# Performance work log

Measured on AMD Instinct MI355X. Metric: run time of the kernel, lower is better.

## Reference

```python
import jax, jax.numpy as jnp
import numpy as np

K = 20
EPS = 1e-5
NEG_SLOPE = 0.2


def knn(x, k):
    # x: [B, C, N] -> idx [B, N, k] of nearest neighbors (negative sq-dist topk)
    inner = -2.0 * jnp.einsum('bcn,bcm->bnm', x, x)
    xx = jnp.sum(x * x, axis=1)  # [B, N]
    d = -xx[:, :, None] - inner - xx[:, None, :]
    return jax.lax.top_k(d, k)[1]


def get_graph_feature(x, k):
    # x: [B, C, N] -> [B, 2C, N, k]
    idx = knn(x, k)
    xt = jnp.transpose(x, (0, 2, 1))            # [B, N, C]
    feat = jax.vmap(lambda a, i: a[i])(xt, idx)  # [B, N, k, C]
    center = xt[:, :, None, :]
    out = jnp.concatenate([feat - center, jnp.broadcast_to(center, feat.shape)], axis=-1)
    return jnp.transpose(out, (0, 3, 1, 2))


def conv_bn_lrelu(x, w, g, b):
    # 1x1 conv + BatchNorm2d (batch stats, training mode) + LeakyReLU(0.2)
    y = jnp.einsum('oc,bcnk->bonk', w, x)
    mu = jnp.mean(y, axis=(0, 2, 3), keepdims=True)
    var = jnp.mean((y - mu) ** 2, axis=(0, 2, 3), keepdims=True)
    y = (y - mu) * jax.lax.rsqrt(var + EPS)
    y = y * g[None, :, None, None] + b[None, :, None, None]
    return jnp.where(y >= 0, y, NEG_SLOPE * y)


def lrelu(y):
    return jnp.where(y >= 0, y, NEG_SLOPE * y)


def setup_inputs() -> dict:
    key = jax.random.key(0)
    ks = jax.random.split(key, 24)
    B, N = 8, 4096
    d = {}
    d['x'] = jax.random.normal(ks[0], (B, 3, N), dtype=jnp.float32)
    def wconv(k_, o, c):
        return jax.random.normal(k_, (o, c), dtype=jnp.float32) * (1.0 / np.sqrt(c))
    d['w1'] = wconv(ks[1], 32, 6)
    d['g1'] = 1.0 + 0.1 * jax.random.normal(ks[2], (32,), dtype=jnp.float32)
    d['b1'] = 0.1 * jax.random.normal(ks[3], (32,), dtype=jnp.float32)
    d['w2'] = wconv(ks[4], 64, 70)
    d['g2'] = 1.0 + 0.1 * jax.random.normal(ks[5], (64,), dtype=jnp.float32)
    d['b2'] = 0.1 * jax.random.normal(ks[6], (64,), dtype=jnp.float32)
    d['wd1'] = wconv(ks[7], 64, 64)
    d['gd1'] = 1.0 + 0.1 * jax.random.normal(ks[8], (64,), dtype=jnp.float32)
    d['bd1'] = 0.1 * jax.random.normal(ks[9], (64,), dtype=jnp.float32)
    d['wd2'] = wconv(ks[10], 64, 128)
    d['gd2'] = 1.0 + 0.1 * jax.random.normal(ks[11], (64,), dtype=jnp.float32)
    d['bd2'] = 0.1 * jax.random.normal(ks[12], (64,), dtype=jnp.float32)
    d['W2d'] = jax.random.normal(ks[13], (128, 128), dtype=jnp.float32) * (1.0 / np.sqrt(128))
    d['b2d'] = 0.1 * jax.random.normal(ks[14], (128,), dtype=jnp.float32)
    d['W3d'] = jax.random.normal(ks[15], (64, 128), dtype=jnp.float32) * (1.0 / np.sqrt(128))
    d['b3d'] = 0.1 * jax.random.normal(ks[16], (64,), dtype=jnp.float32)
    d['W4d'] = jax.random.normal(ks[17], (11, 64), dtype=jnp.float32) * (1.0 / np.sqrt(64))
    d['b4d'] = 0.1 * jax.random.normal(ks[18], (11,), dtype=jnp.float32)
    return d


def reference(x, w1, g1, b1, w2, g2, b2, wd1, gd1, bd1, wd2, gd2, bd2,
              W2d, b2d, W3d, b3d, W4d, b4d):
    x1_gf = get_graph_feature(x, K)                    # [B, 6, N, k]
    x1_max = jnp.max(conv_bn_lrelu(x1_gf, w1, g1, b1), axis=-1)  # [B, 32, N]
    x2_gf = jnp.concatenate([x1_gf, get_graph_feature(x1_max, K)], axis=1)  # [B, 70, N, k]
    x2_max = jnp.max(conv_bn_lrelu(x2_gf, w2, g2, b2), axis=-1)  # [B, 64, N]
    xd1 = jnp.max(conv_bn_lrelu(get_graph_feature(x1_max, K), wd1, gd1, bd1), axis=-1)  # [B, 64, N]
    xd2 = jnp.max(conv_bn_lrelu(get_graph_feature(x2_max, K), wd2, gd2, bd2), axis=-1)  # [B, 64, N]
    h = jnp.concatenate([xd1, xd2], axis=1)            # [B, 128, N]
    h = h.reshape(1, -1, 128)                          # faithful row-major view
    h = jnp.mean(h, axis=1)                            # [1, 128]
    h = lrelu(h @ W2d.T + b2d)
    h = lrelu(h @ W3d.T + b3d)
    return lrelu(h @ W4d.T + b4d)                      # [1, 11]
```

## Files before the change

kernel.cpp:

```cpp
#include <hip/hip_runtime.h>

#define BB 8
#define NN 4096
#define KK 20
constexpr float EPSV = 1e-5f;
constexpr float SLOPE = 0.2f;

typedef __bf16 bfrag __attribute__((ext_vector_type(8)));
typedef float floatx4 __attribute__((ext_vector_type(4)));
typedef unsigned short us4 __attribute__((ext_vector_type(4)));
typedef unsigned short us8 __attribute__((ext_vector_type(8)));

__device__ __forceinline__ float lrelu(float v) { return v >= 0.f ? v : SLOPE * v; }

__device__ __forceinline__ unsigned short bf16rn(float f) {
    unsigned int u = __float_as_uint(f);
    return (unsigned short)((u + 0x7FFFu + ((u >> 16) & 1u)) >> 16);
}
__device__ __forceinline__ float bf16up(unsigned short h) {
    return __uint_as_float(((unsigned int)h) << 16);
}

__device__ __forceinline__ void gl_lds16(const unsigned short* g, unsigned short* l) {
    __builtin_amdgcn_global_load_lds((const __attribute__((address_space(1))) void*)g,
                                     (__attribute__((address_space(3))) void*)l, 16, 0, 0);
}

__global__ void zero_kernel(float* p, int n) {
    int i = blockIdx.x * 256 + threadIdx.x;
    if (i < n) p[i] = 0.f;
}

__global__ void pack3_kernel(const float* __restrict__ src, unsigned short* __restrict__ pk) {
    const int id = blockIdx.x;
    const int b = id & 7;
    const int m = (id >> 3) * 256 + threadIdx.x;
    us8 w0, w1;
    #pragma unroll
    for (int j = 0; j < 8; j++) { w0[j] = 0; w1[j] = 0; }
    unsigned short row[12];
    float s = 0.f;
    #pragma unroll
    for (int c = 0; c < 3; c++) {
        float v = src[(b * 3 + c) * NN + m];
        s += v * v;
        unsigned short h = bf16rn(v);
        unsigned short l = bf16rn(v - bf16up(h));
        row[c] = h; row[3 + c] = l; row[6 + c] = l; row[9 + c] = h;
    }
    #pragma unroll
    for (int j = 0; j < 8; j++) w0[j] = row[j];
    #pragma unroll
    for (int j = 0; j < 4; j++) w1[j] = row[8 + j];
    unsigned short* dst = pk + (size_t)(b * NN + m) * 40;
    us8 z;
    #pragma unroll
    for (int j = 0; j < 8; j++) z[j] = 0;
    unsigned int ub = __float_as_uint(0.5f * s);
    us8 zh = z;
    zh[0] = (unsigned short)(ub & 0xFFFFu);
    zh[1] = (unsigned short)(ub >> 16);
    *(us8*)(dst) = w0;
    *(us8*)(dst + 8) = w1;
    *(us8*)(dst + 16) = z;
    *(us8*)(dst + 24) = z;
    *(us8*)(dst + 32) = zh;
}

template<int C>
__global__ __launch_bounds__(256) void knn_kernel(const float* __restrict__ src,
                                                  const unsigned short* __restrict__ pk,
                                                  int* __restrict__ idx) {
    constexpr int SK = (C == 3) ? 40 : (2 * C + 8);
    constexpr int HNOFF = (C == 3) ? 32 : 2 * C;
    constexpr int UNITS = 8 * SK;
    constexpr int PF = (UNITS + 255) / 256;
    constexpr int KKN = (C == 3) ? 1 : (C / 32);
    __shared__ __attribute__((aligned(16))) unsigned short cpack[2 * 64 * SK];
    __shared__ float pv[64 * 65];
    __shared__ unsigned short pidx[64 * 66];
    __shared__ float tau[64];
    __shared__ int cnt[64];
    __shared__ unsigned short qls[(C == 3) ? 64 * 40 : 2];

    const int bid = blockIdx.x;
    const int b = bid & 7;
    const int q0 = (bid >> 3) * 64;
    const int tid = threadIdx.x;
    const int lane = tid & 63;
    const int wv = tid >> 6;
    const int wr = (wv >> 1) * 32;
    const int wc = (wv & 1) * 32;
    const int fl = lane & 15;
    const int fq = lane >> 4;

    float tv[20]; int ti[20];
    #pragma unroll
    for (int k = 0; k < 20; k++) { tv[k] = -3.4e38f; ti[k] = 0; }

    bfrag qah[KKN][2], qal[KKN][2];
    if (C == 3) {
        for (int i = tid; i < 64 * 20; i += 256) {
            int r = i / 20, k = 12 + i % 20;
            qls[r * 40 + k] = 0;
        }
        if (tid < 64) {
            #pragma unroll
            for (int c = 0; c < 3; c++) {
                float v = src[(b * 3 + c) * NN + q0 + tid];
                unsigned short h = bf16rn(v);
                unsigned short l = bf16rn(v - bf16up(h));
                qls[tid * 40 + c] = h;  qls[tid * 40 + 3 + c] = l;
                qls[tid * 40 + 6 + c] = h;  qls[tid * 40 + 9 + c] = l;
            }
        }
    } else {
        #pragma unroll
        for (int r2 = 0; r2 < 2; r2++) {
            const unsigned short* qr = pk + (size_t)(b * NN + q0 + wr + r2 * 16 + fl) * SK + fq * 8;
            #pragma unroll
            for (int kk = 0; kk < KKN; kk++) {
                qah[kk][r2] = *(const bfrag*)(qr + kk * 32);
                qal[kk][r2] = *(const bfrag*)(qr + C + kk * 32);
            }
        }
    }

    {
        const unsigned short* p0 = pk + (size_t)(b * NN) * SK;
        #pragma unroll
        for (int r = 0; r < PF; r++) {
            int u0 = r * 256 + wv * 64;
            if (u0 < UNITS)
                gl_lds16(p0 + (size_t)(u0 + lane) * 8, cpack + (size_t)u0 * 8);
        }
    }
    if (tid < 64) { tau[tid] = -3.4e38f; cnt[tid] = 0; }
    __syncthreads();

    bfrag qa3[2];
    if (C == 3) {
        #pragma unroll
        for (int r2 = 0; r2 < 2; r2++)
            qa3[r2] = *(const bfrag*)(&qls[(wr + r2 * 16 + fl) * 40 + fq * 8]);
    }

    int buf = 0;
    for (int ch = 0; ch < 64; ch++) {
        unsigned short* cur = cpack + buf * (64 * SK);
        if (ch + 1 < 64) {
            unsigned short* nxt = cpack + (buf ^ 1) * (64 * SK);
            const unsigned short* pn = pk + (size_t)(b * NN + (ch + 1) * 64) * SK;
            #pragma unroll
            for (int r = 0; r < PF; r++) {
                int u0 = r * 256 + wv * 64;
                if (u0 < UNITS)
                    gl_lds16(pn + (size_t)(u0 + lane) * 8, nxt + (size_t)u0 * 8);
            }
        }

        floatx4 acc[2][2];
        #pragma unroll
        for (int r2 = 0; r2 < 2; r2++)
            #pragma unroll
            for (int c2 = 0; c2 < 2; c2++)
                acc[r2][c2] = (floatx4)(0.f);

        if (C == 3) {
            #pragma unroll
            for (int c2 = 0; c2 < 2; c2++) {
                bfrag bm = *(const bfrag*)(&cur[(wc + c2 * 16 + fl) * SK + fq * 8]);
                #pragma unroll
                for (int r2 = 0; r2 < 2; r2++)
                    acc[r2][c2] = __builtin_amdgcn_mfma_f32_16x16x32_bf16(qa3[r2], bm, acc[r2][c2], 0, 0, 0);
            }
        } else {
            #pragma unroll
            for (int kk = 0; kk < KKN; kk++) {
                const int kb = kk * 32 + fq * 8;
                bfrag bh[2], bl[2];
                #pragma unroll
                for (int c2 = 0; c2 < 2; c2++) {
                    bh[c2] = *(const bfrag*)(&cur[(wc + c2 * 16 + fl) * SK + kb]);
                    bl[c2] = *(const bfrag*)(&cur[(wc + c2 * 16 + fl) * SK + C + kb]);
                }
                #pragma unroll
                for (int r2 = 0; r2 < 2; r2++)
                    #pragma unroll
                    for (int c2 = 0; c2 < 2; c2++) {
                        acc[r2][c2] = __builtin_amdgcn_mfma_f32_16x16x32_bf16(qah[kk][r2], bh[c2], acc[r2][c2], 0, 0, 0);
                        acc[r2][c2] = __builtin_amdgcn_mfma_f32_16x16x32_bf16(qah[kk][r2], bl[c2], acc[r2][c2], 0, 0, 0);
                        acc[r2][c2] = __builtin_amdgcn_mfma_f32_16x16x32_bf16(qal[kk][r2], bh[c2], acc[r2][c2], 0, 0, 0);
                        acc[r2][c2] = __builtin_amdgcn_mfma_f32_16x16x32_bf16(qal[kk][r2], bl[c2], acc[r2][c2], 0, 0, 0);
                    }
            }
        }

        {
            const int m0 = ch * 64;
            float hvv[2];
            #pragma unroll
            for (int c2 = 0; c2 < 2; c2++)
                hvv[c2] = *(const float*)(&cur[(wc + c2 * 16 + fl) * SK + HNOFF]);
            #pragma unroll
            for (int r2 = 0; r2 < 2; r2++) {
                const int qb = wr + r2 * 16 + fq * 4;
                float4 t4 = *(const float4*)(&tau[qb]);
                float ta[4] = { t4.x, t4.y, t4.z, t4.w };
                #pragma unroll
                for (int c2 = 0; c2 < 2; c2++) {
                    const float hv = hvv[c2];
                    const int mm = m0 + wc + c2 * 16 + fl;
                    #pragma unroll
                    for (int reg = 0; reg < 4; reg++) {
                        float s = acc[r2][c2][reg] - hv;
                        if (s > ta[reg]) {
                            int q = qb + reg;
                            int p = atomicAdd(&cnt[q], 1);
                            pv[q * 65 + p] = s;
                            pidx[q * 66 + p] = (unsigned short)mm;
                        }
                    }
                }
            }
        }
        __syncthreads();

        if (tid < 64) {
            int n = cnt[tid];
            for (int t = 0; t < n; t++) {
                float v = pv[tid * 65 + t];
                if (v > tv[0]) {
                    tv[0] = v; ti[0] = (int)pidx[tid * 66 + t];
                    #pragma unroll
                    for (int j = 0; j < 19; j++) {
                        if (tv[j] > tv[j + 1]) {
                            float a = tv[j]; tv[j] = tv[j + 1]; tv[j + 1] = a;
                            int bi = ti[j]; ti[j] = ti[j + 1]; ti[j + 1] = bi;
                        }
                    }
                }
            }
            cnt[tid] = 0;
            tau[tid] = tv[0];
        }
        __syncthreads();
        buf ^= 1;
    }

    if (tid < 64) {
        #pragma unroll
        for (int k = 0; k < 20; k++)
            idx[(b * NN + q0 + tid) * KK + k] = ti[k];
    }
}

template<int COUT>
__global__ void precompute_kernel(const float* __restrict__ src, int C,
                                  const float* __restrict__ w, int CIN, int wd_off, int wc_off,
                                  float* __restrict__ G, float* __restrict__ H) {
    constexpr int MY = 256 / COUT;
    extern __shared__ float lds[];
    float* wd = lds;
    float* wc = lds + C * COUT;
    const int id = blockIdx.x;
    const int b = id & 7;
    const int m_base = (id >> 3) * 64;
    const int tid = threadIdx.y * COUT + threadIdx.x;
    for (int i = tid; i < C * COUT; i += 256) {
        int c = i / COUT, o = i % COUT;
        float a  = w[o * CIN + wd_off + c];
        float cc = w[o * CIN + wc_off + c];
        wd[i] = a;
        wc[i] = cc - a;
    }
    __syncthreads();
    const int o = threadIdx.x;
    for (int it = 0; it < COUT / 4; it++) {
        int m = m_base + it * MY + threadIdx.y;
        float g = 0.f, h = 0.f;
        for (int c = 0; c < C; c++) {
            float s = src[(b * C + c) * NN + m];
            g += wd[c * COUT + o] * s;
            h += wc[c * COUT + o] * s;
        }
        int gi = (b * NN + m) * COUT + o;
        G[gi] = g;
        H[gi] = h;
    }
}

__global__ void precompute2_kernel(const float* __restrict__ srcA, const float* __restrict__ srcB,
                                   const float* __restrict__ w,
                                   float* __restrict__ GA, float* __restrict__ GB,
                                   float* __restrict__ H) {
    constexpr int COUT = 64, CA = 3, CB = 32, CIN = 70;
    __shared__ float wdA[CA * COUT], wcA[CA * COUT], wdB[CB * COUT], wcB[CB * COUT];
    const int id = blockIdx.x;
    const int b = id & 7;
    const int m_base = (id >> 3) * 64;
    const int tid = threadIdx.y * COUT + threadIdx.x;
    for (int i = tid; i < CA * COUT; i += 256) {
        int c = i / COUT, o = i % COUT;
        float a = w[o * CIN + 0 + c], cc = w[o * CIN + 3 + c];
        wdA[i] = a; wcA[i] = cc - a;
    }
    for (int i = tid; i < CB * COUT; i += 256) {
        int c = i / COUT, o = i % COUT;
        float a = w[o * CIN + 6 + c], cc = w[o * CIN + 38 + c];
        wdB[i] = a; wcB[i] = cc - a;
    }
    __syncthreads();
    const int o = threadIdx.x;
    for (int it = 0; it < 16; it++) {
        int m = m_base + it * 4 + threadIdx.y;
        float ga = 0.f, gb = 0.f, h = 0.f;
        for (int c = 0; c < CA; c++) {
            float s = srcA[(b * CA + c) * NN + m];
            ga += wdA[c * COUT + o] * s;
            h  += wcA[c * COUT + o] * s;
        }
        for (int c = 0; c < CB; c++) {
            float s = srcB[(b * CB + c) * NN + m];
            gb += wdB[c * COUT + o] * s;
            h  += wcB[c * COUT + o] * s;
        }
        int gi = (b * NN + m) * COUT + o;
        GA[gi] = ga;
        GB[gi] = gb;
        H[gi] = h;
    }
}

template<int COUT, int GROUPS>
__global__ void conv_stats_kernel(const float* __restrict__ G1, const int* __restrict__ idx1,
                                  const float* __restrict__ G2, const int* __restrict__ idx2,
                                  const float* __restrict__ H, const float* __restrict__ gw,
                                  float* __restrict__ stats, float* __restrict__ V) {
    constexpr int NY = 256 / COUT;
    const int id = blockIdx.x;
    const int b = id & 7;
    const int o = threadIdx.x;
    const int n = (id >> 3) * NY + threadIdx.y;
    const int base = b * NN + n;
    const float h = H[base * COUT + o];
    float s1 = 0.f, s2 = 0.f;
    float gx = -3.4e38f, gn = 3.4e38f;
    #pragma unroll
    for (int k = 0; k < KK; k++) {
        int i1 = idx1[base * KK + k];
        float g = G1[(b * NN + i1) * COUT + o];
        if (GROUPS == 2) {
            int i2 = idx2[base * KK + k];
            g += G2[(b * NN + i2) * COUT + o];
        }
        float y = g + h;
        s1 += y;
        s2 += y * y;
        gx = fmaxf(gx, g);
        gn = fminf(gn, g);
    }
    V[base * COUT + o] = ((gw[o] >= 0.f) ? gx : gn) + h;

    __shared__ float ls[2 * COUT];
    if (threadIdx.y == 0) { ls[o] = 0.f; ls[COUT + o] = 0.f; }
    __syncthreads();
    atomicAdd(&ls[o], s1);
    atomicAdd(&ls[COUT + o], s2);
    __syncthreads();
    if (threadIdx.y == 0) {
        atomicAdd(&stats[o], ls[o]);
        atomicAdd(&stats[64 + o], ls[COUT + o]);
    }
}

__global__ void apply_kernel(const float* __restrict__ V, const float* __restrict__ stats,
                             const float* __restrict__ g, const float* __restrict__ bb,
                             float* __restrict__ out, int cout, float invP) {
    const int id = blockIdx.x;
    const int b = id & 7;
    int e = (id >> 3) * 256 + threadIdx.x;
    int n = e & (NN - 1);
    int o = e >> 12;
    __shared__ float sc_s, sh_s;
    if (threadIdx.x == 0) {
        float mu  = stats[o] * invP;
        float var = stats[64 + o] * invP - mu * mu;
        float sc  = g[o] * rsqrtf(var + EPSV);
        sc_s = sc;
        sh_s = bb[o] - mu * sc;
    }
    __syncthreads();
    float v = V[(b * NN + n) * cout + o];
    out[(b * cout + o) * NN + n] = lrelu(sc_s * v + sh_s);
}

template<int COUT>
__global__ void applypack_kernel(const float* __restrict__ V, const float* __restrict__ stats,
                                 const float* __restrict__ g, const float* __restrict__ bb,
                                 float* __restrict__ xm, unsigned short* __restrict__ pk,
                                 float invP) {
    constexpr int SK = 2 * COUT + 8;
    constexpr int Q = COUT / 4;
    __shared__ float sc_s[COUT], sh_s[COUT], hnacc[64];
    const int id = blockIdx.x;
    const int b = id & 7;
    const int m0 = (id >> 3) * 64;
    const int tid = threadIdx.x;
    if (tid < COUT) {
        float mu  = stats[tid] * invP;
        float var = stats[64 + tid] * invP - mu * mu;
        float sc  = g[tid] * rsqrtf(var + EPSV);
        sc_s[tid] = sc;
        sh_s[tid] = bb[tid] - mu * sc;
    }
    if (tid < 64) hnacc[tid] = 0.f;
    __syncthreads();
    const int n = tid & 63;
    const int oc = (tid >> 6) * Q;
    const float* vp = V + ((size_t)(b * NN + m0 + n) * COUT + oc);
    float y[Q];
    float s = 0.f;
    #pragma unroll
    for (int j = 0; j < Q; j++) {
        float yy = lrelu(sc_s[oc + j] * vp[j] + sh_s[oc + j]);
        y[j] = yy;
        s += yy * yy;
        xm[(b * COUT + oc + j) * NN + m0 + n] = yy;
    }
    atomicAdd(&hnacc[n], s);
    unsigned short* pr = pk + (size_t)(b * NN + m0 + n) * SK;
    #pragma unroll
    for (int j4 = 0; j4 < Q / 4; j4++) {
        us4 hv, lv;
        #pragma unroll
        for (int j = 0; j < 4; j++) {
            float yy = y[j4 * 4 + j];
            unsigned short h = bf16rn(yy);
            hv[j] = h;
            lv[j] = bf16rn(yy - bf16up(h));
        }
        *(us4*)(pr + oc + j4 * 4) = hv;
        *(us4*)(pr + COUT + oc + j4 * 4) = lv;
    }
    __syncthreads();
    if (tid < 64)
        *(unsigned int*)(pk + (size_t)(b * NN + m0 + tid) * SK + 2 * COUT) =
            __float_as_uint(0.5f * hnacc[tid]);
}

__global__ void mean_kernel(const float* __restrict__ xd1, const float* __restrict__ xd2,
                            float* __restrict__ hsum) {
    __shared__ float bins[128];
    const int tid = threadIdx.x;
    if (tid < 128) bins[tid] = 0.f;
    __syncthreads();
    const int half = BB * 64 * NN;
    const int stride = gridDim.x * 256;
    for (int e = blockIdx.x * 256 + tid; e < half; e += stride)
        atomicAdd(&bins[e & 127], xd1[e]);
    for (int e = blockIdx.x * 256 + tid; e < half; e += stride)
        atomicAdd(&bins[e & 127], xd2[e]);
    __syncthreads();
    if (tid < 128) atomicAdd(&hsum[tid], bins[tid]);
}

__global__ void head_kernel(const float* __restrict__ hsum,
                            const float* __restrict__ W2d, const float* __restrict__ b2d,
                            const float* __restrict__ W3d, const float* __restrict__ b3d,
                            const float* __restrict__ W4d, const float* __restrict__ b4d,
                            float* __restrict__ out) {
    __shared__ float h[128], t1[128], t2[64];
    const int t = threadIdx.x;
    h[t] = hsum[t] * (1.f / 32768.f);
    __syncthreads();
    float a = b2d[t];
    for (int j = 0; j < 128; j++) a += W2d[t * 128 + j] * h[j];
    t1[t] = lrelu(a);
    __syncthreads();
    if (t < 64) {
        float a2 = b3d[t];
        for (int j = 0; j < 128; j++) a2 += W3d[t * 128 + j] * t1[j];
        t2[t] = lrelu(a2);
    }
    __syncthreads();
    if (t < 11) {
        float a3 = b4d[t];
        for (int j = 0; j < 64; j++) a3 += W4d[t * 64 + j] * t2[j];
        out[t] = lrelu(a3);
    }
}

extern "C" void kernel_launch(void* const* d_in, const int* in_sizes, int n_in,
                              void* d_out, int out_size, void* d_ws, size_t ws_size,
                              hipStream_t stream) {
    const float* x   = (const float*)d_in[0];
    const float* w1  = (const float*)d_in[1];
    const float* g1  = (const float*)d_in[2];
    const float* b1  = (const float*)d_in[3];
    const float* w2  = (const float*)d_in[4];
    const float* g2  = (const float*)d_in[5];
    const float* b2  = (const float*)d_in[6];
    const float* wd1 = (const float*)d_in[7];
    const float* gd1 = (const float*)d_in[8];
    const float* bd1 = (const float*)d_in[9];
    const float* wd2 = (const float*)d_in[10];
    const float* gd2 = (const float*)d_in[11];
    const float* bd2 = (const float*)d_in[12];
    const float* W2d = (const float*)d_in[13];
    const float* b2d = (const float*)d_in[14];
    const float* W3d = (const float*)d_in[15];
    const float* b3d = (const float*)d_in[16];
    const float* W4d = (const float*)d_in[17];
    const float* b4d = (const float*)d_in[18];
    float* out = (float*)d_out;

    char* ws = (char*)d_ws;
    size_t off = 0;
    auto alloc = [&](size_t bytes) { char* p = ws + off; off += (bytes + 255) & ~size_t(255); return p; };
    int*   idx1  = (int*)  alloc(BB * NN * KK * 4);
    int*   idx2  = (int*)  alloc(BB * NN * KK * 4);
    int*   idx3  = (int*)  alloc(BB * NN * KK * 4);
    float* x1m   = (float*)alloc(BB * 32 * NN * 4);
    float* x2m   = (float*)alloc(BB * 64 * NN * 4);
    float* xd1   = (float*)alloc(BB * 64 * NN * 4);
    float* xd2   = (float*)alloc(BB * 64 * NN * 4);
    float* G1    = (float*)alloc((size_t)BB * NN * 64 * 4);
    float* G2    = (float*)alloc((size_t)BB * NN * 64 * 4);
    float* H     = (float*)alloc((size_t)BB * NN * 64 * 4);
    float* Vbuf  = (float*)alloc((size_t)BB * NN * 64 * 4);
    float* stats = (float*)alloc(4 * 256 * 4);
    float* hsum  = (float*)alloc(128 * 4);

    float* st0 = stats;
    float* st1 = stats + 256;
    float* st2 = stats + 512;
    float* st3 = stats + 768;

    unsigned short* pk3  = (unsigned short*)Vbuf;
    unsigned short* pk32 = (unsigned short*)G2;
    unsigned short* pk64 = (unsigned short*)G1;

    const float invP = 1.f / (float)(BB * NN * KK);
    const dim3 knn_grid(NN / 64 * BB);
    const dim3 pre_grid(NN / 64 * BB);

    zero_kernel<<<5, 256, 0, stream>>>(stats, 1024 + 128);

    pack3_kernel<<<NN / 256 * BB, 256, 0, stream>>>(x, pk3);
    knn_kernel<3><<<knn_grid, 256, 0, stream>>>(x, pk3, idx1);

    precompute_kernel<32><<<pre_grid, dim3(32, 8), 2 * 3 * 32 * 4, stream>>>(
        x, 3, w1, 6, 0, 3, G1, H);
    conv_stats_kernel<32, 1><<<NN / 8 * BB, dim3(32, 8), 0, stream>>>(
        G1, idx1, nullptr, nullptr, H, g1, st0, Vbuf);
    applypack_kernel<32><<<pre_grid, 256, 0, stream>>>(Vbuf, st0, g1, b1, x1m, pk32, invP);

    knn_kernel<32><<<knn_grid, 256, 0, stream>>>(x1m, pk32, idx2);

    precompute2_kernel<<<pre_grid, dim3(64, 4), 0, stream>>>(x, x1m, w2, G1, G2, H);
    conv_stats_kernel<64, 2><<<NN / 4 * BB, dim3(64, 4), 0, stream>>>(
        G1, idx1, G2, idx2, H, g2, st1, Vbuf);
    applypack_kernel<64><<<pre_grid, 256, 0, stream>>>(Vbuf, st1, g2, b2, x2m, pk64, invP);

    knn_kernel<64><<<knn_grid, 256, 0, stream>>>(x2m, pk64, idx3);

    precompute_kernel<64><<<pre_grid, dim3(64, 4), 2 * 32 * 64 * 4, stream>>>(
        x1m, 32, wd1, 64, 0, 32, G2, H);
    conv_stats_kernel<64, 1><<<NN / 4 * BB, dim3(64, 4), 0, stream>>>(
        G2, idx2, nullptr, nullptr, H, gd1, st2, Vbuf);
    apply_kernel<<<64 * NN / 256 * BB, 256, 0, stream>>>(Vbuf, st2, gd1, bd1, xd1, 64, invP);

    precompute_kernel<64><<<pre_grid, dim3(64, 4), 2 * 64 * 64 * 4, stream>>>(
        x2m, 64, wd2, 128, 0, 64, G1, H);
    conv_stats_kernel<64, 1><<<NN / 4 * BB, dim3(64, 4), 0, stream>>>(
        G1, idx3, nullptr, nullptr, H, gd2, st3, Vbuf);
    apply_kernel<<<64 * NN / 256 * BB, 256, 0, stream>>>(Vbuf, st3, gd2, bd2, xd2, 64, invP);

    mean_kernel<<<1024, 256, 0, stream>>>(xd1, xd2, hsum);
    head_kernel<<<1, 128, 0, stream>>>(hsum, W2d, b2d, W3d, b3d, W4d, b4d, out);
}
```

Measured before the change: 1.625 ms.

## Fuse dgcnn1 precompute into layer-2 precompute and fold apply into mean reduction

The wd1 precompute now happens inside the layer-2 precompute kernel, because both read x1m. That saves one kernel launch and a second pass over x1m, at the cost of two extra full-size buffers being written. The separate apply and mean kernels are replaced by an applyreduce kernel. It normalises V, applies LeakyReLU and sums over channels with a wave shuffle, then atomically adds into the 128 bins of hsum. This avoids writing and re-reading the xd1/xd2 tensors, but adds global atomics, one per point.

New measurement: 1.822 ms. 1.12x slower.

```diff
diff --git a/kernel.cpp b/kernel.cpp
--- a/kernel.cpp
+++ b/kernel.cpp
@@ -290,45 +290,55 @@
     }
 }
 
-__global__ void precompute2_kernel(const float* __restrict__ srcA, const float* __restrict__ srcB,
-                                   const float* __restrict__ w,
-                                   float* __restrict__ GA, float* __restrict__ GB,
-                                   float* __restrict__ H) {
-    constexpr int COUT = 64, CA = 3, CB = 32, CIN = 70;
-    __shared__ float wdA[CA * COUT], wcA[CA * COUT], wdB[CB * COUT], wcB[CB * COUT];
+__global__ void precompute2x_kernel(const float* __restrict__ srcA, const float* __restrict__ srcB,
+                                    const float* __restrict__ w2, const float* __restrict__ wd1w,
+                                    float* __restrict__ GA, float* __restrict__ GB,
+                                    float* __restrict__ H2,
+                                    float* __restrict__ Gd1, float* __restrict__ Hd1) {
+    constexpr int COUT = 64, CA = 3, CB = 32;
+    __shared__ float wdA[CA * COUT], wcA[CA * COUT];
+    __shared__ float wdB[CB * COUT], wcB[CB * COUT];
+    __shared__ float wdD[CB * COUT], wcD[CB * COUT];
     const int id = blockIdx.x;
     const int b = id & 7;
     const int m_base = (id >> 3) * 64;
     const int tid = threadIdx.y * COUT + threadIdx.x;
     for (int i = tid; i < CA * COUT; i += 256) {
         int c = i / COUT, o = i % COUT;
-        float a = w[o * CIN + 0 + c], cc = w[o * CIN + 3 + c];
+        float a = w2[o * 70 + c], cc = w2[o * 70 + 3 + c];
         wdA[i] = a; wcA[i] = cc - a;
     }
     for (int i = tid; i < CB * COUT; i += 256) {
         int c = i / COUT, o = i % COUT;
-        float a = w[o * CIN + 6 + c], cc = w[o * CIN + 38 + c];
+        float a = w2[o * 70 + 6 + c], cc = w2[o * 70 + 38 + c];
         wdB[i] = a; wcB[i] = cc - a;
+        float ad = wd1w[o * 64 + c], cd = wd1w[o * 64 + 32 + c];
+        wdD[i] = ad; wcD[i] = cd - ad;
     }
     __syncthreads();
     const int o = threadIdx.x;
     for (int it = 0; it < 16; it++) {
         int m = m_base + it * 4 + threadIdx.y;
-        float ga = 0.f, gb = 0.f, h = 0.f;
+        float ga = 0.f, h2 = 0.f;
         for (int c = 0; c < CA; c++) {
             float s = srcA[(b * CA + c) * NN + m];
             ga += wdA[c * COUT + o] * s;
-            h  += wcA[c * COUT + o] * s;
-        }
+            h2 += wcA[c * COUT + o] * s;
+        }
+        float gb = 0.f, gd = 0.f, hd = 0.f;
         for (int c = 0; c < CB; c++) {
             float s = srcB[(b * CB + c) * NN + m];
             gb += wdB[c * COUT + o] * s;
-            h  += wcB[c * COUT + o] * s;
-        }
-        int gi = (b * NN + m) * COUT + o;
+            h2 += wcB[c * COUT + o] * s;
+            gd += wdD[c * COUT + o] * s;
+            hd += wcD[c * COUT + o] * s;
+        }
+        size_t gi = (size_t)(b * NN + m) * COUT + o;
         GA[gi] = ga;
         GB[gi] = gb;
-        H[gi] = h;
+        H2[gi] = h2;
+        Gd1[gi] = gd;
+        Hd1[gi] = hd;
     }
 }
 
@@ -372,27 +382,6 @@
         atomicAdd(&stats[o], ls[o]);
         atomicAdd(&stats[64 + o], ls[COUT + o]);
     }
-}
-
-__global__ void apply_kernel(const float* __restrict__ V, const float* __restrict__ stats,
-                             const float* __restrict__ g, const float* __restrict__ bb,
-                             float* __restrict__ out, int cout, float invP) {
-    const int id = blockIdx.x;
-    const int b = id & 7;
-    int e = (id >> 3) * 256 + threadIdx.x;
-    int n = e & (NN - 1);
-    int o = e >> 12;
-    __shared__ float sc_s, sh_s;
-    if (threadIdx.x == 0) {
-        float mu  = stats[o] * invP;
-        float var = stats[64 + o] * invP - mu * mu;
-        float sc  = g[o] * rsqrtf(var + EPSV);
-        sc_s = sc;
-        sh_s = bb[o] - mu * sc;
-    }
-    __syncthreads();
-    float v = V[(b * NN + n) * cout + o];
-    out[(b * cout + o) * NN + n] = lrelu(sc_s * v + sh_s);
 }
 
 template<int COUT>
@@ -449,20 +438,32 @@
             __float_as_uint(0.5f * hnacc[tid]);
 }
 
-__global__ void mean_kernel(const float* __restrict__ xd1, const float* __restrict__ xd2,
-                            float* __restrict__ hsum) {
-    __shared__ float bins[128];
+__global__ void applyreduce_kernel(const float* __restrict__ V, const float* __restrict__ stats,
+                                   const float* __restrict__ g, const float* __restrict__ bb,
+                                   float* __restrict__ hsum, float invP) {
+    __shared__ float sc_s[64], sh_s[64];
+    const int id = blockIdx.x;
+    const int b = id & 7;
+    const int slice = id >> 3;
     const int tid = threadIdx.x;
-    if (tid < 128) bins[tid] = 0.f;
-    __syncthreads();
-    const int half = BB * 64 * NN;
-    const int stride = gridDim.x * 256;
-    for (int e = blockIdx.x * 256 + tid; e < half; e += stride)
-        atomicAdd(&bins[e & 127], xd1[e]);
-    for (int e = blockIdx.x * 256 + tid; e < half; e += stride)
-        atomicAdd(&bins[e & 127], xd2[e]);
-    __syncthreads();
-    if (tid < 128) atomicAdd(&hsum[tid], bins[tid]);
+    const int o = tid & 63;
+    const int wvn = tid >> 6;
+    if (tid < 64) {
+        float mu  = stats[tid] * invP;
+        float var = stats[64 + tid] * invP - mu * mu;
+        float sc  = g[tid] * rsqrtf(var + EPSV);
+        sc_s[tid] = sc;
+        sh_s[tid] = bb[tid] - mu * sc;
+    }
+    __syncthreads();
+    for (int it = 0; it < 8; it++) {
+        int n = slice * 32 + it * 4 + wvn;
+        float v = V[((size_t)(b * NN + n)) * 64 + o];
+        float y = lrelu(sc_s[o] * v + sh_s[o]);
+        #pragma unroll
+        for (int s = 32; s > 0; s >>= 1) y += __shfl_down(y, s, 64);
+        if (o == 0) atomicAdd(&hsum[n & 127], y);
+    }
 }
 
 __global__ void head_kernel(const float* __restrict__ hsum,
@@ -523,12 +524,12 @@
     int*   idx3  = (int*)  alloc(BB * NN * KK * 4);
     float* x1m   = (float*)alloc(BB * 32 * NN * 4);
     float* x2m   = (float*)alloc(BB * 64 * NN * 4);
-    float* xd1   = (float*)alloc(BB * 64 * NN * 4);
-    float* xd2   = (float*)alloc(BB * 64 * NN * 4);
     float* G1    = (float*)alloc((size_t)BB * NN * 64 * 4);
     float* G2    = (float*)alloc((size_t)BB * NN * 64 * 4);
     float* H     = (float*)alloc((size_t)BB * NN * 64 * 4);
     float* Vbuf  = (float*)alloc((size_t)BB * NN * 64 * 4);
+    float* Gd1   = (float*)alloc((size_t)BB * NN * 64 * 4);
+    float* Hd1   = (float*)alloc((size_t)BB * NN * 64 * 4);
     float* stats = (float*)alloc(4 * 256 * 4);
     float* hsum  = (float*)alloc(128 * 4);
 
@@ -558,25 +559,23 @@
 
     knn_kernel<32><<<knn_grid, 256, 0, stream>>>(x1m, pk32, idx2);
 
-    precompute2_kernel<<<pre_grid, dim3(64, 4), 0, stream>>>(x, x1m, w2, G1, G2, H);
+    precompute2x_kernel<<<pre_grid, dim3(64, 4), 0, stream>>>(
+        x, x1m, w2, wd1, G1, G2, H, Gd1, Hd1);
     conv_stats_kernel<64, 2><<<NN / 4 * BB, dim3(64, 4), 0, stream>>>(
         G1, idx1, G2, idx2, H, g2, st1, Vbuf);
     applypack_kernel<64><<<pre_grid, 256, 0, stream>>>(Vbuf, st1, g2, b2, x2m, pk64, invP);
 
     knn_kernel<64><<<knn_grid, 256, 0, stream>>>(x2m, pk64, idx3);
 
-    precompute_kernel<64><<<pre_grid, dim3(64, 4), 2 * 32 * 64 * 4, stream>>>(
-        x1m, 32, wd1, 64, 0, 32, G2, H);
     conv_stats_kernel<64, 1><<<NN / 4 * BB, dim3(64, 4), 0, stream>>>(
-        G2, idx2, nullptr, nullptr, H, gd1, st2, Vbuf);
-    apply_kernel<<<64 * NN / 256 * BB, 256, 0, stream>>>(Vbuf, st2, gd1, bd1, xd1, 64, invP);
+        Gd1, idx2, nullptr, nullptr, Hd1, gd1, st2, Vbuf);
+    applyreduce_kernel<<<1024, 256, 0, stream>>>(Vbuf, st2, gd1, bd1, hsum, invP);
 
     precompute_kernel<64><<<pre_grid, dim3(64, 4), 2 * 64 * 64 * 4, stream>>>(
         x2m, 64, wd2, 128, 0, 64, G1, H);
     conv_stats_kernel<64, 1><<<NN / 4 * BB, dim3(64, 4), 0, stream>>>(
         G1, idx3, nullptr, nullptr, H, gd2, st3, Vbuf);
-    apply_kernel<<<64 * NN / 256 * BB, 256, 0, stream>>>(Vbuf, st3, gd2, bd2, xd2, 64, invP);
-
-    mean_kernel<<<1024, 256, 0, stream>>>(xd1, xd2, hsum);
+    applyreduce_kernel<<<1024, 256, 0, stream>>>(Vbuf, st3, gd2, bd2, hsum, invP);
+
     head_kernel<<<1, 128, 0, stream>>>(hsum, W2d, b2d, W3d, b3d, W4d, b4d, out);
 }
```
